# Optimization experiments

Measured on AMD Instinct MI355X. Metric: run time of the kernel, lower is better.

The kernel has to match this reference:

```python
import jax, jax.numpy as jnp
import numpy as np

ENC_UNITS = 50
FEAT = 4
T = 100
B = 256


def param_activation(x, min_val, max_val):
    # tanh(x) * scale + min_val + scale, scale = (max-min)/2  -> range (min_val, max_val)
    scale = (max_val - min_val) / 2.0
    return jnp.tanh(x) * scale + min_val + scale


def lstm(x, kernel, rec_kernel, bias):
    # Keras LSTM, gate order i,f,c,o; returns final hidden state h_T. x: [B,T,F]
    u = ENC_UNITS
    # precompute input projections for all timesteps: [B,T,4u]
    zx = jnp.einsum('btf,fg->btg', x, kernel) + bias

    def step(carry, z_t):
        h, c = carry
        z = z_t + h @ rec_kernel  # [B,4u]
        i = jax.nn.sigmoid(z[:, :u])
        f = jax.nn.sigmoid(z[:, u:2 * u])
        g = jnp.tanh(z[:, 2 * u:3 * u])
        o = jax.nn.sigmoid(z[:, 3 * u:])
        c = f * c + i * g
        h = o * jnp.tanh(c)
        return (h, c), None

    h0 = jnp.zeros((x.shape[0], u), x.dtype)
    (h, c), _ = jax.lax.scan(step, (h0, h0), jnp.swapaxes(zx, 0, 1))
    return h


def setup_inputs() -> dict:
    key = jax.random.key(0)
    ks = jax.random.split(key, 16)
    x_scaled = jax.random.normal(ks[0], (B, T, FEAT), dtype=jnp.float32)
    # state: keep vel/dv/dx in a physically sane positive range; dx (channel 3) away from 0
    state = jax.random.uniform(ks[1], (B, T, FEAT), dtype=jnp.float32, minval=1.0, maxval=30.0)
    g = 1.0 / np.sqrt(ENC_UNITS)
    params = {
        'lstm_kernel': jax.random.normal(ks[2], (FEAT, 4 * ENC_UNITS), jnp.float32) * 0.1,
        'lstm_rec_kernel': jax.random.normal(ks[3], (ENC_UNITS, 4 * ENC_UNITS), jnp.float32) * g,
        'lstm_bias': jnp.zeros((4 * ENC_UNITS,), jnp.float32),
        'w_desired_v': jax.random.normal(ks[4], (ENC_UNITS, 1), jnp.float32) * g,
        'b_desired_v': jnp.zeros((1,), jnp.float32),
        'w_desired_tgap': jax.random.normal(ks[5], (ENC_UNITS, 1), jnp.float32) * g,
        'b_desired_tgap': jnp.zeros((1,), jnp.float32),
        'w_min_jamx': jax.random.normal(ks[6], (ENC_UNITS, 1), jnp.float32) * g,
        'b_min_jamx': jnp.ones((1,), jnp.float32),  # keep min_jamx mostly > 0 past relu
        'w_max_act': jax.random.normal(ks[7], (ENC_UNITS, 1), jnp.float32) * g,
        'b_max_act': jnp.zeros((1,), jnp.float32),
        'w_min_act': jax.random.normal(ks[8], (ENC_UNITS, 1), jnp.float32) * g,
        'b_min_act': jnp.zeros((1,), jnp.float32),
    }
    return {'x_scaled': x_scaled, 'state': state, **params}


def reference(x_scaled, state, lstm_kernel, lstm_rec_kernel, lstm_bias,
              w_desired_v, b_desired_v, w_desired_tgap, b_desired_tgap,
              w_min_jamx, b_min_jamx, w_max_act, b_max_act, w_min_act, b_min_act):
    h_t = lstm(x_scaled, lstm_kernel, lstm_rec_kernel, lstm_bias)  # [B, 50]

    desired_v = param_activation(h_t @ w_desired_v + b_desired_v, 15.0, 35.0)     # [B,1]
    desired_tgap = param_activation(h_t @ w_desired_tgap + b_desired_tgap, 0.5, 3.0)
    min_jamx = jax.nn.relu(h_t @ w_min_jamx + b_min_jamx)
    max_act = param_activation(h_t @ w_max_act + b_max_act, 0.5, 3.0)
    min_act = param_activation(h_t @ w_min_act + b_min_act, 0.5, 4.0)
    idm_param = jnp.concatenate([desired_v, desired_tgap, min_jamx, max_act, min_act], axis=1)  # [B,5]

    # Vectorized IDM over all 100 timesteps at once (steps are data-independent).
    vel = state[:, :, 0]  # [B,T]
    dv = state[:, :, 2]
    dx = state[:, :, 3]
    two_sqrt_ab = 2.0 * jnp.sqrt(max_act * min_act)  # [B,1]
    desired_gap = min_jamx + desired_tgap * vel + (vel * dv) / two_sqrt_ab  # [B,T]
    act = max_act * (1.0 - ((vel / desired_v) ** 4.0 + (desired_gap / dx) ** 2.0))  # [B,T]
    act_seq = act[:, :, None]  # [B,T,1]
    return act_seq, idm_param
```

## Files before the change

### kernel.cpp

```cpp
#include <hip/hip_runtime.h>
#include <hip/hip_fp16.h>
#include <math.h>
#include <stdint.h>

#define U 50
#define TT 100
#define BB 256

typedef _Float16 half2v __attribute__((ext_vector_type(2)));

__device__ __forceinline__ float dot2_acc(uint32_t h2, uint32_t w2, float c) {
#if __has_builtin(__builtin_amdgcn_fdot2)
    return __builtin_amdgcn_fdot2(__builtin_bit_cast(half2v, h2),
                                  __builtin_bit_cast(half2v, w2), c, false);
#else
    half2v a = __builtin_bit_cast(half2v, h2);
    half2v b = __builtin_bit_cast(half2v, w2);
    return fmaf((float)a.x, (float)b.x, fmaf((float)a.y, (float)b.y, c));
#endif
}

__device__ __forceinline__ float sigmoid_fast(float x) {
    return 1.0f / (1.0f + __expf(-x));
}
__device__ __forceinline__ float tanh_fast(float x) {
    float e = __expf(2.0f * x);
    return 1.0f - 2.0f / (e + 1.0f);
}
__device__ __forceinline__ float param_act(float x, float mn, float mx) {
    float scale = 0.5f * (mx - mn);
    return tanh_fast(x) * scale + mn + scale;
}

#define BAR() do {                                            \
    asm volatile("s_waitcnt lgkmcnt(0)" ::: "memory");        \
    __builtin_amdgcn_s_barrier();                             \
    asm volatile("" ::: "memory");                            \
} while (0)

__global__ __launch_bounds__(256, 1) void encoder_kernel(
    const float* __restrict__ x,
    const float* __restrict__ state,
    const float* __restrict__ kernel,
    const float* __restrict__ rec,
    const float* __restrict__ bias,
    const float* __restrict__ w_dv, const float* __restrict__ b_dv,
    const float* __restrict__ w_dt, const float* __restrict__ b_dt,
    const float* __restrict__ w_mj, const float* __restrict__ b_mj,
    const float* __restrict__ w_ma, const float* __restrict__ b_ma,
    const float* __restrict__ w_mi, const float* __restrict__ b_mi,
    float* __restrict__ out)
{
    const int b   = blockIdx.x;
    const int tid = threadIdx.x;
    const int w   = tid >> 6;
    const int l   = tid & 63;
    const int cl  = (l < U) ? l : (U - 1);

    __shared__ __align__(16) float4 xlds[TT];
    __shared__ __align__(16) _Float16 h16[64];
    __shared__ float zex[2][4][64];
    __shared__ float idm[8];

    uint32_t wpk[25];
    #pragma unroll
    for (int j = 0; j < 25; ++j) {
        float r0 = rec[(2 * j) * 200 + w * U + cl];
        float r1 = rec[(2 * j + 1) * 200 + w * U + cl];
        half2v p; p.x = (_Float16)r0; p.y = (_Float16)r1;
        wpk[j] = __builtin_bit_cast(uint32_t, p);
    }
    #pragma unroll
    for (int j = 0; j < 25; ++j) asm volatile("" : "+v"(wpk[j]));

    float kc[4];
    #pragma unroll
    for (int f = 0; f < 4; ++f) kc[f] = kernel[f * 200 + w * U + cl];
    float bz = bias[w * U + cl];

    const float4* __restrict__ xg = (const float4*)(x + (size_t)b * TT * 4);
    if (tid < TT) xlds[tid] = xg[tid];
    if (tid < 64) h16[tid] = (_Float16)0.0f;
    __syncthreads();

    float cstate = 0.0f;
    uint32_t hvu[25];
    #pragma unroll
    for (int j = 0; j < 25; ++j) hvu[j] = 0u;

    const uint4* __restrict__ hq = (const uint4*)h16;
    const uint32_t* __restrict__ hd = (const uint32_t*)h16;

    for (int t = 0; t < TT; ++t) {
        float4 x4 = xlds[t];

        float z = fmaf(x4.x, kc[0], fmaf(x4.y, kc[1],
                  fmaf(x4.z, kc[2], fmaf(x4.w, kc[3], bz))));
        float a0 = 0.f, a1 = 0.f;
        #pragma unroll
        for (int j = 0; j < 24; j += 2) {
            a0 = dot2_acc(hvu[j], wpk[j], a0);
            a1 = dot2_acc(hvu[j + 1], wpk[j + 1], a1);
        }
        a0 = dot2_acc(hvu[24], wpk[24], a0);
        z += a0 + a1;

        float nl = (w == 2) ? tanh_fast(z) : sigmoid_fast(z);
        zex[t & 1][w][l] = nl;

        BAR();

        const int buf = t & 1;
        float gi = zex[buf][0][l];
        float gf = zex[buf][1][l];
        float gg = zex[buf][2][l];
        float go = zex[buf][3][l];
        cstate = fmaf(gf, cstate, gi * gg);
        float hn = go * tanh_fast(cstate);
        if (l < U) h16[l] = (_Float16)hn;

        #pragma unroll
        for (int q = 0; q < 6; ++q) {
            uint4 v = hq[q];
            hvu[4 * q + 0] = v.x; hvu[4 * q + 1] = v.y;
            hvu[4 * q + 2] = v.z; hvu[4 * q + 3] = v.w;
        }
        hvu[24] = hd[24];
    }

    if (tid < 5) {
        const float* wv = (tid == 0) ? w_dv : (tid == 1) ? w_dt :
                          (tid == 2) ? w_mj : (tid == 3) ? w_ma : w_mi;
        const float* bv = (tid == 0) ? b_dv : (tid == 1) ? b_dt :
                          (tid == 2) ? b_mj : (tid == 3) ? b_ma : b_mi;
        float s = bv[0];
        #pragma unroll
        for (int j = 0; j < U; ++j) s = fmaf((float)h16[j], wv[j], s);
        float v;
        if (tid == 0)      v = param_act(s, 15.0f, 35.0f);
        else if (tid == 1) v = param_act(s, 0.5f, 3.0f);
        else if (tid == 2) v = fmaxf(s, 0.0f);
        else if (tid == 3) v = param_act(s, 0.5f, 3.0f);
        else               v = param_act(s, 0.5f, 4.0f);
        idm[tid] = v;
        out[BB * TT + b * 5 + tid] = v;
    }
    __syncthreads();

    const float desired_v    = idm[0];
    const float desired_tgap = idm[1];
    const float min_jamx     = idm[2];
    const float max_act      = idm[3];
    const float min_act      = idm[4];
    const float inv_tsab = 1.0f / (2.0f * sqrtf(max_act * min_act));
    const float inv_dv   = 1.0f / desired_v;

    const float4* __restrict__ sb4 = (const float4*)(state + (size_t)b * TT * 4);
    for (int t = tid; t < TT; t += 256) {
        float4 s4 = sb4[t];
        float vel = s4.x;
        float dv  = s4.z;
        float dx  = s4.w;
        float dgap = fmaf(desired_tgap, vel, fmaf(vel * dv, inv_tsab, min_jamx));
        float r1 = vel * inv_dv;
        r1 = r1 * r1;
        r1 = r1 * r1;
        float r2 = dgap / dx;
        r2 = r2 * r2;
        out[b * TT + t] = max_act * (1.0f - (r1 + r2));
    }
}

extern "C" void kernel_launch(void* const* d_in, const int* in_sizes, int n_in,
                              void* d_out, int out_size, void* d_ws, size_t ws_size,
                              hipStream_t stream) {
    const float* x      = (const float*)d_in[0];
    const float* state  = (const float*)d_in[1];
    const float* kern   = (const float*)d_in[2];
    const float* rec    = (const float*)d_in[3];
    const float* bias   = (const float*)d_in[4];
    const float* w_dv   = (const float*)d_in[5];
    const float* b_dv   = (const float*)d_in[6];
    const float* w_dt   = (const float*)d_in[7];
    const float* b_dt   = (const float*)d_in[8];
    const float* w_mj   = (const float*)d_in[9];
    const float* b_mj   = (const float*)d_in[10];
    const float* w_ma   = (const float*)d_in[11];
    const float* b_ma   = (const float*)d_in[12];
    const float* w_mi   = (const float*)d_in[13];
    const float* b_mi   = (const float*)d_in[14];
    float* out = (float*)d_out;

    encoder_kernel<<<BB, 256, 0, stream>>>(
        x, state, kern, rec, bias,
        w_dv, b_dv, w_dt, b_dt, w_mj, b_mj, w_ma, b_ma, w_mi, b_mi,
        out);
}
```

Measured before the change: 44.87 us.

## Process two batch rows per block sharing recurrent weights in registers

Each block now runs two independent LSTM recurrences (two batch elements) interleaved in the same time loop, reusing the packed fp16 recurrent weights held in registers. The grid is halved. The aim is to amortise per-step barrier and LDS latency over two independent dependency chains and to reduce total weight loading. In exchange, per-step ALU work and register pressure double, and only half as many CUs are used.

```diff
diff --git a/kernel.cpp b/kernel.cpp
--- a/kernel.cpp
+++ b/kernel.cpp
@@ -51,16 +51,16 @@
     const float* __restrict__ w_mi, const float* __restrict__ b_mi,
     float* __restrict__ out)
 {
-    const int b   = blockIdx.x;
+    const int bg0 = blockIdx.x * 2;
     const int tid = threadIdx.x;
     const int w   = tid >> 6;
     const int l   = tid & 63;
     const int cl  = (l < U) ? l : (U - 1);
 
-    __shared__ __align__(16) float4 xlds[TT];
-    __shared__ __align__(16) _Float16 h16[64];
-    __shared__ float zex[2][4][64];
-    __shared__ float idm[8];
+    __shared__ __align__(16) float4 xlds[2][TT];
+    __shared__ __align__(16) _Float16 h16[2][64];
+    __shared__ float zex[2][2][4][64];
+    __shared__ float idm[2][8];
 
     uint32_t wpk[25];
     #pragma unroll
@@ -78,96 +78,115 @@
     for (int f = 0; f < 4; ++f) kc[f] = kernel[f * 200 + w * U + cl];
     float bz = bias[w * U + cl];
 
-    const float4* __restrict__ xg = (const float4*)(x + (size_t)b * TT * 4);
-    if (tid < TT) xlds[tid] = xg[tid];
-    if (tid < 64) h16[tid] = (_Float16)0.0f;
+    const float4* __restrict__ xg0 = (const float4*)(x + (size_t)bg0 * TT * 4);
+    const float4* __restrict__ xg1 = (const float4*)(x + (size_t)(bg0 + 1) * TT * 4);
+    if (tid < TT) xlds[0][tid] = xg0[tid];
+    else if (tid < 2 * TT) xlds[1][tid - TT] = xg1[tid - TT];
+    if (tid < 64) { h16[0][tid] = (_Float16)0.0f; h16[1][tid] = (_Float16)0.0f; }
     __syncthreads();
 
-    float cstate = 0.0f;
-    uint32_t hvu[25];
-    #pragma unroll
-    for (int j = 0; j < 25; ++j) hvu[j] = 0u;
-
-    const uint4* __restrict__ hq = (const uint4*)h16;
-    const uint32_t* __restrict__ hd = (const uint32_t*)h16;
+    float cA = 0.0f, cB = 0.0f;
+    uint32_t hva[25], hvb[25];
+    #pragma unroll
+    for (int j = 0; j < 25; ++j) { hva[j] = 0u; hvb[j] = 0u; }
+
+    const uint4* __restrict__ hqA = (const uint4*)&h16[0][0];
+    const uint4* __restrict__ hqB = (const uint4*)&h16[1][0];
+    const uint32_t* __restrict__ hdA = (const uint32_t*)&h16[0][0];
+    const uint32_t* __restrict__ hdB = (const uint32_t*)&h16[1][0];
 
     for (int t = 0; t < TT; ++t) {
-        float4 x4 = xlds[t];
-
-        float z = fmaf(x4.x, kc[0], fmaf(x4.y, kc[1],
-                  fmaf(x4.z, kc[2], fmaf(x4.w, kc[3], bz))));
-        float a0 = 0.f, a1 = 0.f;
+        float4 xa = xlds[0][t];
+        float4 xb = xlds[1][t];
+
+        float zA = fmaf(xa.x, kc[0], fmaf(xa.y, kc[1],
+                   fmaf(xa.z, kc[2], fmaf(xa.w, kc[3], bz))));
+        float zB = fmaf(xb.x, kc[0], fmaf(xb.y, kc[1],
+                   fmaf(xb.z, kc[2], fmaf(xb.w, kc[3], bz))));
+
+        float a0 = 0.f, a1 = 0.f, b0 = 0.f, b1 = 0.f;
         #pragma unroll
         for (int j = 0; j < 24; j += 2) {
-            a0 = dot2_acc(hvu[j], wpk[j], a0);
-            a1 = dot2_acc(hvu[j + 1], wpk[j + 1], a1);
+            a0 = dot2_acc(hva[j],     wpk[j],     a0);
+            b0 = dot2_acc(hvb[j],     wpk[j],     b0);
+            a1 = dot2_acc(hva[j + 1], wpk[j + 1], a1);
+            b1 = dot2_acc(hvb[j + 1], wpk[j + 1], b1);
         }
-        a0 = dot2_acc(hvu[24], wpk[24], a0);
-        z += a0 + a1;
-
-        float nl = (w == 2) ? tanh_fast(z) : sigmoid_fast(z);
-        zex[t & 1][w][l] = nl;
+        a0 = dot2_acc(hva[24], wpk[24], a0);
+        b0 = dot2_acc(hvb[24], wpk[24], b0);
+        zA += a0 + a1;
+        zB += b0 + b1;
+
+        float nlA = (w == 2) ? tanh_fast(zA) : sigmoid_fast(zA);
+        float nlB = (w == 2) ? tanh_fast(zB) : sigmoid_fast(zB);
+        const int buf = t & 1;
+        zex[0][buf][w][l] = nlA;
+        zex[1][buf][w][l] = nlB;
 
         BAR();
 
-        const int buf = t & 1;
-        float gi = zex[buf][0][l];
-        float gf = zex[buf][1][l];
-        float gg = zex[buf][2][l];
-        float go = zex[buf][3][l];
-        cstate = fmaf(gf, cstate, gi * gg);
-        float hn = go * tanh_fast(cstate);
-        if (l < U) h16[l] = (_Float16)hn;
+        float giA = zex[0][buf][0][l], gfA = zex[0][buf][1][l];
+        float ggA = zex[0][buf][2][l], goA = zex[0][buf][3][l];
+        float giB = zex[1][buf][0][l], gfB = zex[1][buf][1][l];
+        float ggB = zex[1][buf][2][l], goB = zex[1][buf][3][l];
+        cA = fmaf(gfA, cA, giA * ggA);
+        cB = fmaf(gfB, cB, giB * ggB);
+        float hnA = goA * tanh_fast(cA);
+        float hnB = goB * tanh_fast(cB);
+        if (l < U) h16[0][l] = (_Float16)hnA;
+        if (l < U) h16[1][l] = (_Float16)hnB;
 
         #pragma unroll
         for (int q = 0; q < 6; ++q) {
-            uint4 v = hq[q];
-            hvu[4 * q + 0] = v.x; hvu[4 * q + 1] = v.y;
-            hvu[4 * q + 2] = v.z; hvu[4 * q + 3] = v.w;
+            uint4 vA = hqA[q];
+            uint4 vB = hqB[q];
+            hva[4 * q + 0] = vA.x; hva[4 * q + 1] = vA.y;
+            hva[4 * q + 2] = vA.z; hva[4 * q + 3] = vA.w;
+            hvb[4 * q + 0] = vB.x; hvb[4 * q + 1] = vB.y;
+            hvb[4 * q + 2] = vB.z; hvb[4 * q + 3] = vB.w;
         }
-        hvu[24] = hd[24];
-    }
-
-    if (tid < 5) {
-        const float* wv = (tid == 0) ? w_dv : (tid == 1) ? w_dt :
-                          (tid == 2) ? w_mj : (tid == 3) ? w_ma : w_mi;
-        const float* bv = (tid == 0) ? b_dv : (tid == 1) ? b_dt :
-                          (tid == 2) ? b_mj : (tid == 3) ? b_ma : b_mi;
+        hva[24] = hdA[24];
+        hvb[24] = hdB[24];
+    }
+
+    if (tid < 10) {
+        const int bi = tid / 5, head = tid % 5;
+        const float* wv = (head == 0) ? w_dv : (head == 1) ? w_dt :
+                          (head == 2) ? w_mj : (head == 3) ? w_ma : w_mi;
+        const float* bv = (head == 0) ? b_dv : (head == 1) ? b_dt :
+                          (head == 2) ? b_mj : (head == 3) ? b_ma : b_mi;
         float s = bv[0];
         #pragma unroll
-        for (int j = 0; j < U; ++j) s = fmaf((float)h16[j], wv[j], s);
+        for (int j = 0; j < U; ++j) s = fmaf((float)h16[bi][j], wv[j], s);
         float v;
-        if (tid == 0)      v = param_act(s, 15.0f, 35.0f);
-        else if (tid == 1) v = param_act(s, 0.5f, 3.0f);
-        else if (tid == 2) v = fmaxf(s, 0.0f);
-        else if (tid == 3) v = param_act(s, 0.5f, 3.0f);
-        else               v = param_act(s, 0.5f, 4.0f);
-        idm[tid] = v;
-        out[BB * TT + b * 5 + tid] = v;
+        if (head == 0)      v = param_act(s, 15.0f, 35.0f);
+        else if (head == 1) v = param_act(s, 0.5f, 3.0f);
+        else if (head == 2) v = fmaxf(s, 0.0f);
+        else if (head == 3) v = param_act(s, 0.5f, 3.0f);
+        else                v = param_act(s, 0.5f, 4.0f);
+        idm[bi][head] = v;
+        out[BB * TT + (bg0 + bi) * 5 + head] = v;
     }
     __syncthreads();
 
-    const float desired_v    = idm[0];
-    const float desired_tgap = idm[1];
-    const float min_jamx     = idm[2];
-    const float max_act      = idm[3];
-    const float min_act      = idm[4];
-    const float inv_tsab = 1.0f / (2.0f * sqrtf(max_act * min_act));
-    const float inv_dv   = 1.0f / desired_v;
-
-    const float4* __restrict__ sb4 = (const float4*)(state + (size_t)b * TT * 4);
-    for (int t = tid; t < TT; t += 256) {
-        float4 s4 = sb4[t];
-        float vel = s4.x;
-        float dv  = s4.z;
-        float dx  = s4.w;
+    if (tid < 2 * TT) {
+        const int bi = tid / TT, t = tid % TT;
+        const int bg = bg0 + bi;
+        const float desired_v    = idm[bi][0];
+        const float desired_tgap = idm[bi][1];
+        const float min_jamx     = idm[bi][2];
+        const float max_act      = idm[bi][3];
+        const float min_act      = idm[bi][4];
+        const float inv_tsab = 1.0f / (2.0f * sqrtf(max_act * min_act));
+        const float inv_dv   = 1.0f / desired_v;
+        float4 s4 = ((const float4*)(state + (size_t)bg * TT * 4))[t];
+        float vel = s4.x, dv = s4.z, dx = s4.w;
         float dgap = fmaf(desired_tgap, vel, fmaf(vel * dv, inv_tsab, min_jamx));
         float r1 = vel * inv_dv;
-        r1 = r1 * r1;
-        r1 = r1 * r1;
+        r1 = r1 * r1; r1 = r1 * r1;
         float r2 = dgap / dx;
         r2 = r2 * r2;
-        out[b * TT + t] = max_act * (1.0f - (r1 + r2));
+        out[bg * TT + t] = max_act * (1.0f - (r1 + r2));
     }
 }
 
@@ -191,7 +210,7 @@
     const float* b_mi   = (const float*)d_in[14];
     float* out = (float*)d_out;
 
-    encoder_kernel<<<BB, 256, 0, stream>>>(
+    encoder_kernel<<<BB / 2, 256, 0, stream>>>(
         x, state, kern, rec, bias,
         w_dv, b_dv, w_dt, b_dt, w_mj, b_mj, w_ma, b_ma, w_mi, b_mi,
         out);
```

Result: slower. 77.64 us (+73.0%).

## Compute all four gates per unit with quad-split dot products and DPP reduction

Applied to the files above, without the earlier changes.

Reassigns work so each group of four lanes owns one hidden unit. Each lane computes partial dot products for all four gates over a quarter of the reduction dimension, and the partials are combined with DPP quad sums. The input projection and bias are folded into the recurrent matvec by appending x_t and a constant 1 to the fp16 h buffer. That buffer is double-buffered so each step needs a single barrier and no cross-wave gate exchange through LDS. This also moves x and bias weights to fp16 and trades per-lane independent accumulator chains for extra DPP shuffles.

```diff
diff --git a/kernel.cpp b/kernel.cpp
--- a/kernel.cpp
+++ b/kernel.cpp
@@ -32,11 +32,29 @@
     return tanh_fast(x) * scale + mn + scale;
 }
 
+__device__ __forceinline__ float quad_sum(float v) {
+    int a = __builtin_amdgcn_mov_dpp(__builtin_bit_cast(int, v), 0xB1, 0xF, 0xF, true);
+    float s = v + __builtin_bit_cast(float, a);
+    int b = __builtin_amdgcn_mov_dpp(__builtin_bit_cast(int, s), 0x4E, 0xF, 0xF, true);
+    return s + __builtin_bit_cast(float, b);
+}
+
 #define BAR() do {                                            \
     asm volatile("s_waitcnt lgkmcnt(0)" ::: "memory");        \
     __builtin_amdgcn_s_barrier();                             \
     asm volatile("" ::: "memory");                            \
 } while (0)
+
+__device__ __forceinline__ float welem(const float* __restrict__ rec,
+                                       const float* __restrict__ kern,
+                                       const float* __restrict__ bias,
+                                       int unit, int g, int j) {
+    if (unit >= U) return 0.0f;
+    if (j < U)      return rec[j * 200 + g * U + unit];
+    if (j < U + 4)  return kern[(j - U) * 200 + g * U + unit];
+    if (j == U + 4) return bias[g * U + unit];
+    return 0.0f;
+}
 
 __global__ __launch_bounds__(256, 1) void encoder_kernel(
     const float* __restrict__ x,
@@ -55,78 +73,90 @@
     const int tid = threadIdx.x;
     const int w   = tid >> 6;
     const int l   = tid & 63;
-    const int cl  = (l < U) ? l : (U - 1);
+    const int kq  = l & 3;
+    const int ul  = l >> 2;
+    const int unit = 16 * w + ul;
 
     __shared__ __align__(16) float4 xlds[TT];
-    __shared__ __align__(16) _Float16 h16[64];
-    __shared__ float zex[2][4][64];
+    __shared__ __align__(16) _Float16 hbuf[2][64];
     __shared__ float idm[8];
 
-    uint32_t wpk[25];
+    uint32_t wpk[4][8];
     #pragma unroll
-    for (int j = 0; j < 25; ++j) {
-        float r0 = rec[(2 * j) * 200 + w * U + cl];
-        float r1 = rec[(2 * j + 1) * 200 + w * U + cl];
-        half2v p; p.x = (_Float16)r0; p.y = (_Float16)r1;
-        wpk[j] = __builtin_bit_cast(uint32_t, p);
+    for (int g = 0; g < 4; ++g) {
+        #pragma unroll
+        for (int p = 0; p < 8; ++p) {
+            const int jj = 2 * (8 * kq + p);
+            float f0 = welem(rec, kernel, bias, unit, g, jj);
+            float f1 = welem(rec, kernel, bias, unit, g, jj + 1);
+            half2v pk; pk.x = (_Float16)f0; pk.y = (_Float16)f1;
+            wpk[g][p] = __builtin_bit_cast(uint32_t, pk);
+        }
     }
     #pragma unroll
-    for (int j = 0; j < 25; ++j) asm volatile("" : "+v"(wpk[j]));
-
-    float kc[4];
-    #pragma unroll
-    for (int f = 0; f < 4; ++f) kc[f] = kernel[f * 200 + w * U + cl];
-    float bz = bias[w * U + cl];
-
-    const float4* __restrict__ xg = (const float4*)(x + (size_t)b * TT * 4);
-    if (tid < TT) xlds[tid] = xg[tid];
-    if (tid < 64) h16[tid] = (_Float16)0.0f;
+    for (int g = 0; g < 4; ++g)
+        #pragma unroll
+        for (int p = 0; p < 8; ++p) asm volatile("" : "+v"(wpk[g][p]));
+
+    if (tid < TT) xlds[tid] = ((const float4*)(x + (size_t)b * TT * 4))[tid];
+    if (tid < 64) {
+        _Float16 v0 = (_Float16)0.0f, v1 = (_Float16)0.0f;
+        if (tid >= U && tid < U + 4)
+            v0 = (_Float16)x[(size_t)b * TT * 4 + (tid - U)];
+        if (tid == U + 4) { v0 = (_Float16)1.0f; v1 = (_Float16)1.0f; }
+        hbuf[0][tid] = v0;
+        hbuf[1][tid] = v1;
+    }
     __syncthreads();
 
     float cstate = 0.0f;
-    uint32_t hvu[25];
-    #pragma unroll
-    for (int j = 0; j < 25; ++j) hvu[j] = 0u;
-
-    const uint4* __restrict__ hq = (const uint4*)h16;
-    const uint32_t* __restrict__ hd = (const uint32_t*)h16;
+    float hT = 0.0f;
 
     for (int t = 0; t < TT; ++t) {
-        float4 x4 = xlds[t];
-
-        float z = fmaf(x4.x, kc[0], fmaf(x4.y, kc[1],
-                  fmaf(x4.z, kc[2], fmaf(x4.w, kc[3], bz))));
-        float a0 = 0.f, a1 = 0.f;
-        #pragma unroll
-        for (int j = 0; j < 24; j += 2) {
-            a0 = dot2_acc(hvu[j], wpk[j], a0);
-            a1 = dot2_acc(hvu[j + 1], wpk[j + 1], a1);
+        const int rb = t & 1, wb = rb ^ 1;
+
+        const uint4* hb = (const uint4*)&hbuf[rb][0];
+        uint4 q0 = hb[2 * kq + 0];
+        uint4 q1 = hb[2 * kq + 1];
+        uint32_t hv[8] = {q0.x, q0.y, q0.z, q0.w, q1.x, q1.y, q1.z, q1.w};
+
+        float4 xn = {0.f, 0.f, 0.f, 0.f};
+        if (tid == 0) xn = xlds[(t + 1 < TT) ? (t + 1) : t];
+
+        float za[4] = {0.f, 0.f, 0.f, 0.f};
+        float zb[4] = {0.f, 0.f, 0.f, 0.f};
+        #pragma unroll
+        for (int p = 0; p < 8; p += 2) {
+            #pragma unroll
+            for (int g = 0; g < 4; ++g) {
+                za[g] = dot2_acc(hv[p],     wpk[g][p],     za[g]);
+                zb[g] = dot2_acc(hv[p + 1], wpk[g][p + 1], zb[g]);
+            }
         }
-        a0 = dot2_acc(hvu[24], wpk[24], a0);
-        z += a0 + a1;
-
-        float nl = (w == 2) ? tanh_fast(z) : sigmoid_fast(z);
-        zex[t & 1][w][l] = nl;
-
-        BAR();
-
-        const int buf = t & 1;
-        float gi = zex[buf][0][l];
-        float gf = zex[buf][1][l];
-        float gg = zex[buf][2][l];
-        float go = zex[buf][3][l];
+
+        float z0 = quad_sum(za[0] + zb[0]);
+        float z1 = quad_sum(za[1] + zb[1]);
+        float z2 = quad_sum(za[2] + zb[2]);
+        float z3 = quad_sum(za[3] + zb[3]);
+
+        float gi = sigmoid_fast(z0);
+        float gf = sigmoid_fast(z1);
+        float gg = tanh_fast(z2);
+        float go = sigmoid_fast(z3);
         cstate = fmaf(gf, cstate, gi * gg);
         float hn = go * tanh_fast(cstate);
-        if (l < U) h16[l] = (_Float16)hn;
-
-        #pragma unroll
-        for (int q = 0; q < 6; ++q) {
-            uint4 v = hq[q];
-            hvu[4 * q + 0] = v.x; hvu[4 * q + 1] = v.y;
-            hvu[4 * q + 2] = v.z; hvu[4 * q + 3] = v.w;
+        hT = hn;
+        if (kq == 0 && unit < U) hbuf[wb][unit] = (_Float16)hn;
+        if (tid == 0) {
+            half2v p0; p0.x = (_Float16)xn.x; p0.y = (_Float16)xn.y;
+            half2v p1; p1.x = (_Float16)xn.z; p1.y = (_Float16)xn.w;
+            *(uint32_t*)&hbuf[wb][U]     = __builtin_bit_cast(uint32_t, p0);
+            *(uint32_t*)&hbuf[wb][U + 2] = __builtin_bit_cast(uint32_t, p1);
         }
-        hvu[24] = hd[24];
-    }
+
+        BAR();
+    }
+    (void)hT;
 
     if (tid < 5) {
         const float* wv = (tid == 0) ? w_dv : (tid == 1) ? w_dt :
@@ -135,7 +165,7 @@
                           (tid == 2) ? b_mj : (tid == 3) ? b_ma : b_mi;
         float s = bv[0];
         #pragma unroll
-        for (int j = 0; j < U; ++j) s = fmaf((float)h16[j], wv[j], s);
+        for (int j = 0; j < U; ++j) s = fmaf((float)hbuf[0][j], wv[j], s);
         float v;
         if (tid == 0)      v = param_act(s, 15.0f, 35.0f);
         else if (tid == 1) v = param_act(s, 0.5f, 3.0f);
@@ -147,27 +177,22 @@
     }
     __syncthreads();
 
-    const float desired_v    = idm[0];
-    const float desired_tgap = idm[1];
-    const float min_jamx     = idm[2];
-    const float max_act      = idm[3];
-    const float min_act      = idm[4];
-    const float inv_tsab = 1.0f / (2.0f * sqrtf(max_act * min_act));
-    const float inv_dv   = 1.0f / desired_v;
-
-    const float4* __restrict__ sb4 = (const float4*)(state + (size_t)b * TT * 4);
-    for (int t = tid; t < TT; t += 256) {
-        float4 s4 = sb4[t];
-        float vel = s4.x;
-        float dv  = s4.z;
-        float dx  = s4.w;
+    if (tid < TT) {
+        const float desired_v    = idm[0];
+        const float desired_tgap = idm[1];
+        const float min_jamx     = idm[2];
+        const float max_act      = idm[3];
+        const float min_act      = idm[4];
+        const float inv_tsab = 1.0f / (2.0f * sqrtf(max_act * min_act));
+        const float inv_dv   = 1.0f / desired_v;
+        float4 s4 = ((const float4*)(state + (size_t)b * TT * 4))[tid];
+        float vel = s4.x, dv = s4.z, dx = s4.w;
         float dgap = fmaf(desired_tgap, vel, fmaf(vel * dv, inv_tsab, min_jamx));
         float r1 = vel * inv_dv;
-        r1 = r1 * r1;
-        r1 = r1 * r1;
+        r1 = r1 * r1; r1 = r1 * r1;
         float r2 = dgap / dx;
         r2 = r2 * r2;
-        out[b * TT + t] = max_act * (1.0f - (r1 + r2));
+        out[b * TT + tid] = max_act * (1.0f - (r1 + r2));
     }
 }
 
```

Result: slower. 57.71 us (+28.6%).

## Split recurrent dot-product K dimension across two wave groups per block

Applied to the files above, without the earlier changes.

Each block now uses 512 threads. Two groups of four waves each compute a partial recurrent dot product over half of the hidden units, which halves the serial dot2 chain per timestep. Partial sums are exchanged through shared memory, and the gate nonlinearities move after the barrier, where every wave evaluates all four gates redundantly. In exchange the kernel does more LDS traffic and more transcendental work per step, and barriers now span 8 waves.

```diff
diff --git a/kernel.cpp b/kernel.cpp
--- a/kernel.cpp
+++ b/kernel.cpp
@@ -6,6 +6,7 @@
 #define U 50
 #define TT 100
 #define BB 256
+#define SPLIT 12
 
 typedef _Float16 half2v __attribute__((ext_vector_type(2)));
 
@@ -38,7 +39,7 @@
     asm volatile("" ::: "memory");                            \
 } while (0)
 
-__global__ __launch_bounds__(256, 1) void encoder_kernel(
+__global__ __launch_bounds__(512, 2) void encoder_kernel(
     const float* __restrict__ x,
     const float* __restrict__ state,
     const float* __restrict__ kernel,
@@ -54,78 +55,101 @@
     const int b   = blockIdx.x;
     const int tid = threadIdx.x;
     const int w   = tid >> 6;
+    const int g   = w & 3;
+    const int kh  = w >> 2;
     const int l   = tid & 63;
     const int cl  = (l < U) ? l : (U - 1);
 
     __shared__ __align__(16) float4 xlds[TT];
     __shared__ __align__(16) _Float16 h16[64];
-    __shared__ float zex[2][4][64];
+    __shared__ float zpart[2][8][64];
     __shared__ float idm[8];
 
-    uint32_t wpk[25];
+    const int p0 = kh ? SPLIT : 0;
+    const int np = kh ? (25 - SPLIT) : SPLIT;
+    uint32_t wpk[13];
     #pragma unroll
-    for (int j = 0; j < 25; ++j) {
-        float r0 = rec[(2 * j) * 200 + w * U + cl];
-        float r1 = rec[(2 * j + 1) * 200 + w * U + cl];
-        half2v p; p.x = (_Float16)r0; p.y = (_Float16)r1;
-        wpk[j] = __builtin_bit_cast(uint32_t, p);
-    }
-    #pragma unroll
-    for (int j = 0; j < 25; ++j) asm volatile("" : "+v"(wpk[j]));
+    for (int j = 0; j < 13; ++j) {
+        float r0 = 0.0f, r1 = 0.0f;
+        if (j < np) {
+            const int p = p0 + j;
+            r0 = rec[(2 * p) * 200 + g * U + cl];
+            r1 = rec[(2 * p + 1) * 200 + g * U + cl];
+        }
+        half2v pk; pk.x = (_Float16)r0; pk.y = (_Float16)r1;
+        wpk[j] = __builtin_bit_cast(uint32_t, pk);
+    }
 
     float kc[4];
     #pragma unroll
-    for (int f = 0; f < 4; ++f) kc[f] = kernel[f * 200 + w * U + cl];
-    float bz = bias[w * U + cl];
-
-    const float4* __restrict__ xg = (const float4*)(x + (size_t)b * TT * 4);
-    if (tid < TT) xlds[tid] = xg[tid];
+    for (int f = 0; f < 4; ++f) kc[f] = kernel[f * 200 + g * U + cl];
+    float bz = bias[g * U + cl];
+
+    if (tid < TT) xlds[tid] = ((const float4*)(x + (size_t)b * TT * 4))[tid];
     if (tid < 64) h16[tid] = (_Float16)0.0f;
     __syncthreads();
 
     float cstate = 0.0f;
-    uint32_t hvu[25];
+    uint32_t hv[13];
     #pragma unroll
-    for (int j = 0; j < 25; ++j) hvu[j] = 0u;
+    for (int j = 0; j < 13; ++j) hv[j] = 0u;
 
     const uint4* __restrict__ hq = (const uint4*)h16;
     const uint32_t* __restrict__ hd = (const uint32_t*)h16;
 
     for (int t = 0; t < TT; ++t) {
-        float4 x4 = xlds[t];
-
-        float z = fmaf(x4.x, kc[0], fmaf(x4.y, kc[1],
-                  fmaf(x4.z, kc[2], fmaf(x4.w, kc[3], bz))));
-        float a0 = 0.f, a1 = 0.f;
-        #pragma unroll
-        for (int j = 0; j < 24; j += 2) {
-            a0 = dot2_acc(hvu[j], wpk[j], a0);
-            a1 = dot2_acc(hvu[j + 1], wpk[j + 1], a1);
+        const int buf = t & 1;
+
+        float p;
+        if (kh == 0) {
+            float4 x4 = xlds[t];
+            p = fmaf(x4.x, kc[0], fmaf(x4.y, kc[1],
+                fmaf(x4.z, kc[2], fmaf(x4.w, kc[3], bz))));
+            float a0 = 0.f, a1 = 0.f;
+            #pragma unroll
+            for (int j = 0; j < 12; j += 2) {
+                a0 = dot2_acc(hv[j],     wpk[j],     a0);
+                a1 = dot2_acc(hv[j + 1], wpk[j + 1], a1);
+            }
+            p += a0 + a1;
+        } else {
+            float a0 = 0.f, a1 = 0.f;
+            #pragma unroll
+            for (int j = 0; j < 12; j += 2) {
+                a0 = dot2_acc(hv[j],     wpk[j],     a0);
+                a1 = dot2_acc(hv[j + 1], wpk[j + 1], a1);
+            }
+            a0 = dot2_acc(hv[12], wpk[12], a0);
+            p = a0 + a1;
         }
-        a0 = dot2_acc(hvu[24], wpk[24], a0);
-        z += a0 + a1;
-
-        float nl = (w == 2) ? tanh_fast(z) : sigmoid_fast(z);
-        zex[t & 1][w][l] = nl;
+        zpart[buf][w][l] = p;
 
         BAR();
 
-        const int buf = t & 1;
-        float gi = zex[buf][0][l];
-        float gf = zex[buf][1][l];
-        float gg = zex[buf][2][l];
-        float go = zex[buf][3][l];
+        float z0 = zpart[buf][0][l] + zpart[buf][4][l];
+        float z1 = zpart[buf][1][l] + zpart[buf][5][l];
+        float z2 = zpart[buf][2][l] + zpart[buf][6][l];
+        float z3 = zpart[buf][3][l] + zpart[buf][7][l];
+        float gi = sigmoid_fast(z0);
+        float gf = sigmoid_fast(z1);
+        float gg = tanh_fast(z2);
+        float go = sigmoid_fast(z3);
         cstate = fmaf(gf, cstate, gi * gg);
         float hn = go * tanh_fast(cstate);
         if (l < U) h16[l] = (_Float16)hn;
 
-        #pragma unroll
-        for (int q = 0; q < 6; ++q) {
-            uint4 v = hq[q];
-            hvu[4 * q + 0] = v.x; hvu[4 * q + 1] = v.y;
-            hvu[4 * q + 2] = v.z; hvu[4 * q + 3] = v.w;
+        if (kh == 0) {
+            uint4 q0 = hq[0], q1 = hq[1], q2 = hq[2];
+            hv[0] = q0.x; hv[1] = q0.y; hv[2]  = q0.z; hv[3]  = q0.w;
+            hv[4] = q1.x; hv[5] = q1.y; hv[6]  = q1.z; hv[7]  = q1.w;
+            hv[8] = q2.x; hv[9] = q2.y; hv[10] = q2.z; hv[11] = q2.w;
+        } else {
+            uint4 q0 = hq[3], q1 = hq[4], q2 = hq[5];
+            hv[0] = q0.x; hv[1] = q0.y; hv[2]  = q0.z; hv[3]  = q0.w;
+            hv[4] = q1.x; hv[5] = q1.y; hv[6]  = q1.z; hv[7]  = q1.w;
+            hv[8] = q2.x; hv[9] = q2.y; hv[10] = q2.z; hv[11] = q2.w;
+            hv[12] = hd[24];
         }
-        hvu[24] = hd[24];
     }
 
     if (tid < 5) {
@@ -147,27 +171,22 @@
     }
     __syncthreads();
 
-    const float desired_v    = idm[0];
-    const float desired_tgap = idm[1];
-    const float min_jamx     = idm[2];
-    const float max_act      = idm[3];
-    const float min_act      = idm[4];
-    const float inv_tsab = 1.0f / (2.0f * sqrtf(max_act * min_act));
-    const float inv_dv   = 1.0f / desired_v;
-
-    const float4* __restrict__ sb4 = (const float4*)(state + (size_t)b * TT * 4);
-    for (int t = tid; t < TT; t += 256) {
-        float4 s4 = sb4[t];
-        float vel = s4.x;
-        float dv  = s4.z;
-        float dx  = s4.w;
+    if (tid < TT) {
+        const float desired_v    = idm[0];
+        const float desired_tgap = idm[1];
+        const float min_jamx     = idm[2];
+        const float max_act      = idm[3];
+        const float min_act      = idm[4];
+        const float inv_tsab = 1.0f / (2.0f * sqrtf(max_act * min_act));
+        const float inv_dv   = 1.0f / desired_v;
+        float4 s4 = ((const float4*)(state + (size_t)b * TT * 4))[tid];
+        float vel = s4.x, dv = s4.z, dx = s4.w;
         float dgap = fmaf(desired_tgap, vel, fmaf(vel * dv, inv_tsab, min_jamx));
         float r1 = vel * inv_dv;
-        r1 = r1 * r1;
-        r1 = r1 * r1;
+        r1 = r1 * r1; r1 = r1 * r1;
         float r2 = dgap / dx;
         r2 = r2 * r2;
-        out[b * TT + t] = max_act * (1.0f - (r1 + r2));
+        out[b * TT + tid] = max_act * (1.0f - (r1 + r2));
     }
 }
 
@@ -191,7 +210,7 @@
     const float* b_mi   = (const float*)d_in[14];
     float* out = (float*)d_out;
 
-    encoder_kernel<<<BB, 256, 0, stream>>>(
+    encoder_kernel<<<BB, 512, 0, stream>>>(
         x, state, kern, rec, bias,
         w_dv, b_dv, w_dt, b_dt, w_mj, b_mj, w_ma, b_ma, w_mi, b_mi,
         out);
```

Result: slower. 74.37 us (+65.7%).
